# Kernel optimization log

Hardware: AMD Instinct MI355X
Metric: run time of the kernel (lower is better)

Reference implementation:

```python
import jax, jax.numpy as jnp
import numpy as np
from jax import lax

B, N, T, NX = 4, 512, 24, 8
H = 64
PRED_LEN, NY = 12, 1
E_RAND = 8192
EPS = 1e-5


def setup_inputs() -> dict:
    key = jax.random.key(0)
    ks = jax.random.split(key, 24)
    sc = lambda k, shape: (jax.random.normal(k, shape, jnp.float32) * 0.05)
    x = jax.random.normal(ks[0], (B, N, T, NX), jnp.float32)
    er = jax.random.randint(ks[1], (2, E_RAND), 0, N, dtype=jnp.int32)
    loops = jnp.stack([jnp.arange(N, dtype=jnp.int32), jnp.arange(N, dtype=jnp.int32)])
    edge_index = jnp.concatenate([er, loops], axis=1)  # [2, 8704]
    return {
        'x': x,
        'edge_index': edge_index,
        'W_fc': sc(ks[2], (NX, H)), 'b_fc': jnp.zeros((H,), jnp.float32),
        'W1': sc(ks[3], (H, H)), 'a_l1': sc(ks[4], (H,)), 'a_r1': sc(ks[5], (H,)), 'bias1': jnp.zeros((H,), jnp.float32),
        'W2': sc(ks[6], (H, H)), 'a_l2': sc(ks[7], (H,)), 'a_r2': sc(ks[8], (H,)), 'bias2': jnp.zeros((H,), jnp.float32),
        'W_ih': sc(ks[9], (4 * H, H)), 'W_hh': sc(ks[10], (4 * H, H)),
        'b_ih': jnp.zeros((4 * H,), jnp.float32), 'b_hh': jnp.zeros((4 * H,), jnp.float32),
        'g_l': jnp.ones((H,), jnp.float32), 'b_l': jnp.zeros((H,), jnp.float32),
        'g_g': jnp.ones((H,), jnp.float32), 'b_g': jnp.zeros((H,), jnp.float32),
        'W_d': sc(ks[11], (H, PRED_LEN * NY)), 'b_d': jnp.zeros((PRED_LEN * NY,), jnp.float32),
    }


def _layer_norm(x, g, b):
    mu = jnp.mean(x, axis=-1, keepdims=True)
    var = jnp.mean(jnp.square(x - mu), axis=-1, keepdims=True)
    return (x - mu) * lax.rsqrt(var + EPS) * g + b


def _gat(x, W, a_l, a_r, bias, mask):
    # x: [B,N,T,F] -> operate in [B,T,N,H] layout (torch transpose(1,2))
    h = jnp.einsum('bntf,fh->btnh', x, W)          # [B,T,N,H]
    el = jnp.einsum('btnh,h->btn', h, a_l)          # attn_l
    er = jnp.einsum('btnh,h->btn', h, a_r)          # attn_r
    e = el[..., :, None] + er[..., None, :]         # [B,T,N,N]
    e = jax.nn.leaky_relu(e, negative_slope=0.2)
    e = jnp.where(mask, e, -jnp.inf)
    alpha = jax.nn.softmax(e, axis=-1)
    out = jnp.einsum('btmn,btnh->bmth', alpha, h) + bias  # back to [B,N,T,H]
    return jax.nn.gelu(out, approximate=False)


def _lstm(xseq, W_ih, W_hh, b_ih, b_hh):
    # xseq: [M, T, H] -> outputs [M, T, H]; PyTorch gate order i,f,g,o
    M = xseq.shape[0]
    Hh = W_hh.shape[1]
    b = b_ih + b_hh
    def step(carry, xt):
        hprev, cprev = carry
        gates = xt @ W_ih.T + hprev @ W_hh.T + b
        i, f, g, o = jnp.split(gates, 4, axis=-1)
        c = jax.nn.sigmoid(f) * cprev + jax.nn.sigmoid(i) * jnp.tanh(g)
        h = jax.nn.sigmoid(o) * jnp.tanh(c)
        return (h, c), h
    init = (jnp.zeros((M, Hh), xseq.dtype), jnp.zeros((M, Hh), xseq.dtype))
    _, hs = lax.scan(step, init, xseq.transpose(1, 0, 2))  # [T,M,H]
    return hs.transpose(1, 0, 2)


def reference(x, edge_index, W_fc, b_fc, W1, a_l1, a_r1, bias1, W2, a_l2, a_r2, bias2,
              W_ih, W_hh, b_ih, b_hh, g_l, b_l, g_g, b_g, W_d, b_d):
    Bb, Nn, Tt, _ = x.shape
    mask = jnp.zeros((Nn, Nn), bool).at[edge_index[0], edge_index[1]].set(True)
    x_h = jnp.einsum('bntf,fh->bnth', x, W_fc) + b_fc          # fc
    g1 = _gat(x_h, W1, a_l1, a_r1, bias1, mask)                # conv1
    g2 = _gat(g1, W2, a_l2, a_r2, bias2, mask)                 # conv2
    l = _lstm(x_h.reshape(Bb * Nn, Tt, -1), W_ih, W_hh, b_ih, b_hh).reshape(Bb, Nn, Tt, -1)
    h = _layer_norm(g2, g_g, b_g) + _layer_norm(l, g_l, b_l)
    last = h[:, :, -1, :]                                       # [B,N,H]
    out = last @ W_d + b_d                                      # [B,N,pred_len*ny]
    return out.reshape(Bb, Nn, PRED_LEN, NY)
```

## Files before the change

### kernel.cpp

```cpp
#include <hip/hip_runtime.h>
#include <hip/hip_bf16.h>
#include <math.h>

#define BB 4
#define NN 512
#define TT 24
#define NXF 8
#define HH 64
#define PRED 12
#define MM (BB*NN)

typedef __attribute__((ext_vector_type(8))) short short8;
typedef __attribute__((ext_vector_type(4))) float f32x4;
typedef unsigned short ushort;

#define WS_H1THI   0
#define WS_H1TLO   65536
#define WS_H2THI   131072
#define WS_H2TLO   196608
#define WS_HL      262144
#define WS_EL      393216
#define WS_ER      395264
#define WS_EL2     397312
#define WS_ER2     399360
#define WS_WCOMB   401408
#define WS_BCOMB   403456
#define WS_WHHFRAG 403712

#define LHS 72
#define LXS 40

__device__ inline float sigm(float x){ return 1.f/(1.f+__expf(-x)); }
__device__ inline float tanh_fast(float x){ float e=__expf(2.f*x); return 1.f - 2.f/(e+1.f); }
__device__ inline float gelu_exact(float x){ return 0.5f*x*(1.f+erff(x*0.70710678118654752440f)); }
__device__ inline ushort f2bu(float f){
    unsigned b=__float_as_uint(f);
    return (ushort)((b + 0x7FFFu + ((b>>16)&1u))>>16);
}
__device__ inline float bu2f(ushort u){ return __uint_as_float(((unsigned)u)<<16); }

__device__ inline void split8(const float* f, short8& hi, short8& lo){
    #pragma unroll
    for (int j = 0; j < 8; ++j){
        ushort h = f2bu(f[j]);
        hi[j] = (short)h;
        lo[j] = (short)f2bu(f[j] - bu2f(h));
    }
}

__global__ __launch_bounds__(256,2) void gat1pre_kernel(
    const float* __restrict__ x, const float* __restrict__ Wfc, const float* __restrict__ bfc,
    const float* __restrict__ W1, const float* __restrict__ al1, const float* __restrict__ ar1,
    const float* __restrict__ Wih, const float* __restrict__ Whh,
    const float* __restrict__ bih, const float* __restrict__ bhh,
    ushort* __restrict__ H1Thi, ushort* __restrict__ H1Tlo,
    float* __restrict__ el, float* __restrict__ er,
    float* __restrict__ wcombG, float* __restrict__ bcombG,
    ushort* __restrict__ whhfrag)
{
    __shared__ float sw1[HH*HH];
    __shared__ float swfc[NXF*HH];
    __shared__ float sb[HH], sal[HH], sar[HH];
    __shared__ float sxh[4][68];
    __shared__ float sx[4][NXF];
    const int t = threadIdx.x;

    if (blockIdx.x >= 512){
        const int f = blockIdx.x - 512;
        const int ng = t;
        float accf = 0.f, accb = 0.f;
        const float* wr = Wih + ng*64;
        #pragma unroll
        for (int k = 0; k < 64; ++k){
            float wv = wr[k];
            accf += Wfc[f*64 + k] * wv;
            accb += bfc[k] * wv;
        }
        wcombG[f*256 + ng] = accf;
        if (f == 0) bcombG[ng] = accb + bih[ng] + bhh[ng];
        #pragma unroll
        for (int u = 0; u < 8; ++u){
            int o = f*2048 + u*256 + t;
            int F  = o >> 9;
            int ln = (o >> 3) & 63;
            int j  = o & 7;
            int w_ = F >> 3, tt = (F >> 1) & 3, ks = F & 1;
            int q = ln >> 4, c = ln & 15;
            int ngx = (w_ + 4*tt)*16 + c;
            whhfrag[o] = f2bu(Whh[ngx*64 + ks*32 + q*8 + j]);
        }
        return;
    }

    const int r = t >> 6, h = t & 63;
    #pragma unroll
    for (int i = 0; i < 16; ++i) sw1[t + 256*i] = W1[t + 256*i];
    swfc[t] = Wfc[t];
    swfc[t+256] = Wfc[t+256];
    if (t < 64) sb[t] = bfc[t];
    else if (t < 128) sal[t-64] = al1[t-64];
    else if (t < 192) sar[t-128] = ar1[t-128];
    if (t < 32){
        int rr = t >> 3, f = t & 7;
        sx[rr][f] = x[(size_t)(blockIdx.x*4 + rr)*(TT*NXF) + (TT-1)*NXF + f];
    }
    __syncthreads();
    float xh = sb[h];
    #pragma unroll
    for (int f = 0; f < NXF; ++f) xh += sx[r][f]*swfc[f*HH + h];
    sxh[r][h] = xh;
    __syncthreads();
    float acc = 0.f;
    const float4* xr = (const float4*)&sxh[r][0];
    #pragma unroll
    for (int k4 = 0; k4 < 16; ++k4){
        float4 xv = xr[k4];
        acc += xv.x*sw1[(4*k4+0)*HH+h] + xv.y*sw1[(4*k4+1)*HH+h]
             + xv.z*sw1[(4*k4+2)*HH+h] + xv.w*sw1[(4*k4+3)*HH+h];
    }
    const int m = blockIdx.x*4 + r;
    {
        int bb = m >> 9, ml = m & 511;
        ushort hu = f2bu(acc);
        H1Thi[((size_t)(bb*HH + h))*NN + ml] = hu;
        H1Tlo[((size_t)(bb*HH + h))*NN + ml] = f2bu(acc - bu2f(hu));
    }
    float v1 = acc*sal[h], v2 = acc*sar[h];
    #pragma unroll
    for (int o = 32; o; o >>= 1){ v1 += __shfl_xor(v1,o); v2 += __shfl_xor(v2,o); }
    if (h == 0){ el[m] = v1; er[m] = v2; }
}

__global__ __launch_bounds__(256,2) void mid_fused_kernel(
    const ushort* __restrict__ H1Thi, const ushort* __restrict__ H1Tlo,
    const float* __restrict__ el_in, const float* __restrict__ er_in,
    const int* __restrict__ ei, int E,
    const float* __restrict__ bias1,
    const float* __restrict__ W2, const float* __restrict__ al2, const float* __restrict__ ar2,
    ushort* __restrict__ H2Thi, ushort* __restrict__ H2Tlo,
    float* __restrict__ el2, float* __restrict__ er2,
    const float* __restrict__ x,
    const float* __restrict__ wcombG, const float* __restrict__ bcombG,
    const ushort* __restrict__ whhfrag,
    float* __restrict__ hl)
{
    __shared__ __align__(16) char smem[58880];
    const int t = threadIdx.x;
    const int lane = t & 63;
    const int w = t >> 6;
    const int quad = lane >> 4;
    const int c16 = lane & 15;

    if (blockIdx.x >= 128){
        ushort* hbi = (ushort*)smem;
        ushort* hlo = (ushort*)(smem + 4608);
        ushort* xls = (ushort*)(smem + 9216);
        const int m0 = (blockIdx.x - 128) * 16;

        {
            unsigned* h0 = (unsigned*)hbi;
            unsigned* l0 = (unsigned*)hlo;
            for (int i = t; i < 2*16*LHS/2; i += 256){ h0[i] = 0u; l0[i] = 0u; }
            unsigned* xw = (unsigned*)xls;
            for (int i = t; i < TT*16*LXS/2; i += 256) xw[i] = 0u;
        }
        short8 bw[4][2]; short8 bx[4]; float bc[4];
        #pragma unroll
        for (int tt = 0; tt < 4; ++tt){
            const int ng = (w + 4*tt)*16 + c16;
            bc[tt] = bcombG[ng];
            #pragma unroll
            for (int ks = 0; ks < 2; ++ks)
                bw[tt][ks] = *(const short8*)&whhfrag[(((w*4+tt)*2)+ks)*512 + lane*8];
            short8 vx = {0,0,0,0,0,0,0,0};
            if (quad == 0){
                #pragma unroll
                for (int j = 0; j < 8; ++j) vx[j] = (short)f2bu(wcombG[j*256 + ng]);
            }
            bx[tt] = vx;
        }
        __syncthreads();
        for (int i = t; i < 16*TT*NXF; i += 256){
            int r = i / (TT*NXF);
            int rem = i - r*(TT*NXF);
            int st = rem >> 3, f = rem & 7;
            xls[st*(16*LXS) + r*LXS + f] = f2bu(x[(size_t)(m0+r)*(TT*NXF) + rem]);
        }
        __syncthreads();

        float cst[4] = {0,0,0,0};
        float hf[4]  = {0,0,0,0};

        for (int st = 0; st < TT; ++st){
            const int p = st & 1;
            const ushort* hb  = hbi + p*(16*LHS);
            const ushort* hl_ = hlo + p*(16*LHS);
            short8 ahi0 = *(const short8*)&hb[c16*LHS + quad*8];
            short8 ahi1 = *(const short8*)&hb[c16*LHS + 32 + quad*8];
            short8 alo0 = *(const short8*)&hl_[c16*LHS + quad*8];
            short8 alo1 = *(const short8*)&hl_[c16*LHS + 32 + quad*8];
            short8 ax   = *(const short8*)&xls[st*(16*LXS) + c16*LXS + quad*8];
            f32x4 acc[4];
            #pragma unroll
            for (int tt = 0; tt < 4; ++tt){
                f32x4 a = {bc[tt], bc[tt], bc[tt], bc[tt]};
                a = __builtin_amdgcn_mfma_f32_16x16x32_bf16(ax,   bx[tt],    a, 0,0,0);
                a = __builtin_amdgcn_mfma_f32_16x16x32_bf16(ahi0, bw[tt][0], a, 0,0,0);
                a = __builtin_amdgcn_mfma_f32_16x16x32_bf16(ahi1, bw[tt][1], a, 0,0,0);
                a = __builtin_amdgcn_mfma_f32_16x16x32_bf16(alo0, bw[tt][0], a, 0,0,0);
                a = __builtin_amdgcn_mfma_f32_16x16x32_bf16(alo1, bw[tt][1], a, 0,0,0);
                acc[tt] = a;
            }
            ushort* ho   = hbi + (p^1)*(16*LHS);
            ushort* lo_o = hlo + (p^1)*(16*LHS);
            #pragma unroll
            for (int reg = 0; reg < 4; ++reg){
                float gi = acc[0][reg], gf = acc[1][reg], gg = acc[2][reg], go = acc[3][reg];
                float cn = sigm(gf)*cst[reg] + sigm(gi)*tanh_fast(gg);
                cst[reg] = cn;
                float hn = sigm(go)*tanh_fast(cn);
                hf[reg] = hn;
                ushort hu = f2bu(hn);
                float lov = hn - bu2f(hu);
                int addr = (quad*4+reg)*LHS + w*16 + c16;
                ho[addr] = hu;
                lo_o[addr] = f2bu(lov);
            }
            __syncthreads();
        }
        #pragma unroll
        for (int reg = 0; reg < 4; ++reg)
            hl[(size_t)(m0 + quad*4 + reg)*HH + w*16 + c16] = hf[reg];
        return;
    }

    unsigned (*smask)[16] = (unsigned(*)[16])smem;
    float* er_s  = (float*)(smem + 1024);
    float* sal   = (float*)(smem + 3072);
    float* sar   = (float*)(smem + 3328);
    float (*alpha)[516] = (float(*)[516])(smem + 3584);
    float* uSpace = (float*)(smem + 36608);
    float (*xh2)[68] = (float(*)[68])(smem + 54528);

    const int b = blockIdx.x >> 5;
    const int m0 = (blockIdx.x & 31) * 16;
    const int l = lane;

    if (t < 64) sal[t] = al2[t]; else if (t < 128) sar[t-64] = ar2[t-64];
    ((unsigned*)smask)[t] = 0;
    er_s[t] = er_in[b*NN + t];
    er_s[t+256] = er_in[b*NN + t + 256];
    __syncthreads();
    for (int e = t; e < E; e += 256){
        int s = ei[e];
        unsigned rl = (unsigned)(s - m0);
        if (rl < 16u){
            int d = ei[E + e];
            atomicOr(&smask[rl][d>>5], 1u << (d & 31));
        }
    }
    __syncthreads();
    for (int q = 0; q < 4; ++q){
        const int i = w*4 + q;
        const float elv = el_in[b*NN + m0 + i];
        float e8[8]; unsigned mk = 0; float mx = -1e30f;
        #pragma unroll
        for (int j = 0; j < 8; ++j){
            int n = l + 64*j;
            float ev = elv + er_s[n];
            ev = ev >= 0.f ? ev : 0.2f*ev;
            unsigned mb = (smask[i][(l>>5) + 2*j] >> (l & 31)) & 1u;
            e8[j] = ev;
            if (mb){ mk |= (1u<<j); mx = fmaxf(mx, ev); }
        }
        #pragma unroll
        for (int o = 32; o; o >>= 1) mx = fmaxf(mx, __shfl_xor(mx, o));
        float s = 0.f;
        #pragma unroll
        for (int j = 0; j < 8; ++j){
            float p = ((mk>>j) & 1u) ? __expf(e8[j]-mx) : 0.f;
            e8[j] = p; s += p;
        }
        #pragma unroll
        for (int o = 32; o; o >>= 1) s += __shfl_xor(s, o);
        const float inv = 1.f/s;
        #pragma unroll
        for (int j = 0; j < 8; ++j) alpha[i][l + 64*j] = e8[j]*inv;
    }
    __syncthreads();

    const ushort* bhp = H1Thi + ((size_t)(b*HH + w*16 + c16))*NN;
    const ushort* blp = H1Tlo + ((size_t)(b*HH + w*16 + c16))*NN;
    f32x4 acc = {0.f,0.f,0.f,0.f};
    for (int k0 = 0; k0 < NN; k0 += 32){
        const float* ap = &alpha[c16][k0 + quad*8];
        float4 a0 = *(const float4*)ap;
        float4 a1 = *(const float4*)(ap + 4);
        float af[8] = {a0.x,a0.y,a0.z,a0.w,a1.x,a1.y,a1.z,a1.w};
        short8 a_h, a_l;
        split8(af, a_h, a_l);
        short8 b_h = *(const short8*)&bhp[k0 + quad*8];
        short8 b_l = *(const short8*)&blp[k0 + quad*8];
        acc = __builtin_amdgcn_mfma_f32_16x16x32_bf16(a_h, b_h, acc, 0,0,0);
        acc = __builtin_amdgcn_mfma_f32_16x16x32_bf16(a_l, b_h, acc, 0,0,0);
        acc = __builtin_amdgcn_mfma_f32_16x16x32_bf16(a_h, b_l, acc, 0,0,0);
    }
    __syncthreads();
    {
        const int h = w*16 + c16;
        const float bv = bias1[h];
        #pragma unroll
        for (int reg = 0; reg < 4; ++reg)
            xh2[quad*4 + reg][h] = gelu_exact(acc[reg] + bv);
    }
    float* sw2 = uSpace;
    #pragma unroll
    for (int i = 0; i < 16; ++i) sw2[t + 256*i] = W2[t + 256*i];
    __syncthreads();
    {
        const int h = l;
        for (int q = 0; q < 4; ++q){
            const int i = w + 4*q;
            float acc2 = 0.f;
            const float4* xr = (const float4*)&xh2[i][0];
            #pragma unroll
            for (int k4 = 0; k4 < 16; ++k4){
                float4 xv = xr[k4];
                acc2 += xv.x*sw2[(4*k4+0)*HH+h] + xv.y*sw2[(4*k4+1)*HH+h]
                      + xv.z*sw2[(4*k4+2)*HH+h] + xv.w*sw2[(4*k4+3)*HH+h];
            }
            const int m = b*NN + m0 + i;
            ushort hu = f2bu(acc2);
            H2Thi[((size_t)(b*HH + h))*NN + (m0 + i)] = hu;
            H2Tlo[((size_t)(b*HH + h))*NN + (m0 + i)] = f2bu(acc2 - bu2f(hu));
            float v1 = acc2*sal[h], v2 = acc2*sar[h];
            #pragma unroll
            for (int o = 32; o; o >>= 1){ v1 += __shfl_xor(v1,o); v2 += __shfl_xor(v2,o); }
            if (h == 0){ el2[m] = v1; er2[m] = v2; }
        }
    }
}

__global__ __launch_bounds__(256,2) void attn2_final_kernel(
    const ushort* __restrict__ H2Thi, const ushort* __restrict__ H2Tlo,
    const float* __restrict__ el_in, const float* __restrict__ er_in,
    const int* __restrict__ ei, int E,
    const float* __restrict__ bias2,
    const float* __restrict__ hl,
    const float* __restrict__ g_l, const float* __restrict__ b_l,
    const float* __restrict__ g_g, const float* __restrict__ b_g,
    const float* __restrict__ W_d, const float* __restrict__ b_d,
    float* __restrict__ out)
{
    __shared__ __align__(16) char smem[54016];
    unsigned (*smask)[16] = (unsigned(*)[16])smem;
    float* er_s  = (float*)(smem + 1024);
    float (*alpha)[516] = (float(*)[516])(smem + 3072);

    const int t = threadIdx.x;
    const int b = blockIdx.x >> 5;
    const int m0 = (blockIdx.x & 31) * 16;
    const int l = t & 63, w = t >> 6;
    const int quad = l >> 4, c16 = l & 15;

    ((unsigned*)smask)[t] = 0;
    er_s[t] = er_in[b*NN + t];
    er_s[t+256] = er_in[b*NN + t + 256];
    __syncthreads();
    for (int e = t; e < E; e += 256){
        int s = ei[e];
        unsigned rl = (unsigned)(s - m0);
        if (rl < 16u){
            int d = ei[E + e];
            atomicOr(&smask[rl][d>>5], 1u << (d & 31));
        }
    }
    __syncthreads();
    for (int q = 0; q < 4; ++q){
        const int i = w*4 + q;
        const float elv = el_in[b*NN + m0 + i];
        float e8[8]; unsigned mk = 0; float mx = -1e30f;
        #pragma unroll
        for (int j = 0; j < 8; ++j){
            int n = l + 64*j;
            float ev = elv + er_s[n];
            ev = ev >= 0.f ? ev : 0.2f*ev;
            unsigned mb = (smask[i][(l>>5) + 2*j] >> (l & 31)) & 1u;
            e8[j] = ev;
            if (mb){ mk |= (1u<<j); mx = fmaxf(mx, ev); }
        }
        #pragma unroll
        for (int o = 32; o; o >>= 1) mx = fmaxf(mx, __shfl_xor(mx, o));
        float s = 0.f;
        #pragma unroll
        for (int j = 0; j < 8; ++j){
            float p = ((mk>>j) & 1u) ? __expf(e8[j]-mx) : 0.f;
            e8[j] = p; s += p;
        }
        #pragma unroll
        for (int o = 32; o; o >>= 1) s += __shfl_xor(s, o);
        const float inv = 1.f/s;
        #pragma unroll
        for (int j = 0; j < 8; ++j) alpha[i][l + 64*j] = e8[j]*inv;
    }
    __syncthreads();

    const ushort* bhp = H2Thi + ((size_t)(b*HH + w*16 + c16))*NN;
    const ushort* blp = H2Tlo + ((size_t)(b*HH + w*16 + c16))*NN;
    f32x4 acc = {0.f,0.f,0.f,0.f};
    for (int k0 = 0; k0 < NN; k0 += 32){
        const float* ap = &alpha[c16][k0 + quad*8];
        float4 a0 = *(const float4*)ap;
        float4 a1 = *(const float4*)(ap + 4);
        float af[8] = {a0.x,a0.y,a0.z,a0.w,a1.x,a1.y,a1.z,a1.w};
        short8 a_h, a_l;
        split8(af, a_h, a_l);
        short8 b_h = *(const short8*)&bhp[k0 + quad*8];
        short8 b_l = *(const short8*)&blp[k0 + quad*8];
        acc = __builtin_amdgcn_mfma_f32_16x16x32_bf16(a_h, b_h, acc, 0,0,0);
        acc = __builtin_amdgcn_mfma_f32_16x16x32_bf16(a_l, b_h, acc, 0,0,0);
        acc = __builtin_amdgcn_mfma_f32_16x16x32_bf16(a_h, b_l, acc, 0,0,0);
    }
    __syncthreads();
    float* sg2  = (float*)(smem + 3072);
    float* sdec = (float*)(smem + 36096);
    {
        const int h = w*16 + c16;
        const float bv = bias2[h];
        #pragma unroll
        for (int reg = 0; reg < 4; ++reg)
            sg2[(quad*4 + reg)*HH + h] = gelu_exact(acc[reg] + bv);
    }
    __syncthreads();
    const int gbase = b*NN + m0;
    {
        const int h = l;
        for (int q = 0; q < 4; ++q){
            const int ml = w*4 + q;
            float gv = sg2[ml*HH + h];
            float lv = hl[(size_t)(gbase + ml)*HH + h];

            float s1 = gv;
            #pragma unroll
            for (int o = 32; o; o >>= 1) s1 += __shfl_xor(s1, o);
            float dg = gv - s1*(1.f/64.f);
            float v1 = dg*dg;
            #pragma unroll
            for (int o = 32; o; o >>= 1) v1 += __shfl_xor(v1, o);
            float lng = dg*rsqrtf(v1*(1.f/64.f) + 1e-5f)*g_g[h] + b_g[h];

            float s2 = lv;
            #pragma unroll
            for (int o = 32; o; o >>= 1) s2 += __shfl_xor(s2, o);
            float dl = lv - s2*(1.f/64.f);
            float v2 = dl*dl;
            #pragma unroll
            for (int o = 32; o; o >>= 1) v2 += __shfl_xor(v2, o);
            float lnl = dl*rsqrtf(v2*(1.f/64.f) + 1e-5f)*g_l[h] + b_l[h];

            sdec[ml*HH + h] = lng + lnl;
        }
    }
    __syncthreads();
    if (t < 16*PRED){
        int rr = t / PRED, pp = t - rr*PRED;
        float a = b_d[pp];
        #pragma unroll
        for (int k = 0; k < HH; ++k) a += sdec[rr*HH + k]*W_d[k*PRED + pp];
        out[(size_t)(gbase + rr)*PRED + pp] = a;
    }
}

extern "C" void kernel_launch(void* const* d_in, const int* in_sizes, int n_in,
                              void* d_out, int out_size, void* d_ws, size_t ws_size,
                              hipStream_t stream){
    const float* x    = (const float*)d_in[0];
    const int*   ei   = (const int*)  d_in[1];
    const float* Wfc  = (const float*)d_in[2];
    const float* bfc  = (const float*)d_in[3];
    const float* W1   = (const float*)d_in[4];
    const float* al1  = (const float*)d_in[5];
    const float* ar1  = (const float*)d_in[6];
    const float* bias1= (const float*)d_in[7];
    const float* W2   = (const float*)d_in[8];
    const float* al2  = (const float*)d_in[9];
    const float* ar2  = (const float*)d_in[10];
    const float* bias2= (const float*)d_in[11];
    const float* Wih  = (const float*)d_in[12];
    const float* Whh  = (const float*)d_in[13];
    const float* bih  = (const float*)d_in[14];
    const float* bhh  = (const float*)d_in[15];
    const float* g_l  = (const float*)d_in[16];
    const float* b_l  = (const float*)d_in[17];
    const float* g_g  = (const float*)d_in[18];
    const float* b_g  = (const float*)d_in[19];
    const float* W_d  = (const float*)d_in[20];
    const float* b_d  = (const float*)d_in[21];

    float* ws = (float*)d_ws;
    const int E = in_sizes[1] / 2;

    gat1pre_kernel<<<512 + 8, 256, 0, stream>>>(x, Wfc, bfc, W1, al1, ar1,
                                                Wih, Whh, bih, bhh,
                                                (ushort*)(ws+WS_H1THI), (ushort*)(ws+WS_H1TLO),
                                                ws+WS_EL, ws+WS_ER,
                                                ws+WS_WCOMB, ws+WS_BCOMB,
                                                (ushort*)(ws+WS_WHHFRAG));
    mid_fused_kernel<<<256, 256, 0, stream>>>((const ushort*)(ws+WS_H1THI), (const ushort*)(ws+WS_H1TLO),
                                              ws+WS_EL, ws+WS_ER,
                                              ei, E, bias1, W2, al2, ar2,
                                              (ushort*)(ws+WS_H2THI), (ushort*)(ws+WS_H2TLO),
                                              ws+WS_EL2, ws+WS_ER2,
                                              x, ws+WS_WCOMB, ws+WS_BCOMB,
                                              (const ushort*)(ws+WS_WHHFRAG),
                                              ws+WS_HL);
    attn2_final_kernel<<<BB*(NN/16), 256, 0, stream>>>((const ushort*)(ws+WS_H2THI), (const ushort*)(ws+WS_H2TLO),
                                                       ws+WS_EL2, ws+WS_ER2,
                                                       ei, E, bias2,
                                                       ws+WS_HL,
                                                       g_l, b_l, g_g, b_g, W_d, b_d,
                                                       (float*)d_out);
}
```

Baseline: 151.2 us.

## Merge three kernels into one cooperative kernel with grid syncs

Replaces the three separate launches (GAT1 projection, mid-stage LSTM/attention, final attention and decoder) with a single cooperative mega-kernel of 256 blocks that uses grid.sync between phases. The first phase now handles 8 rows per block, and the last 8 blocks also precompute the combined LSTM weights. The aim is to remove kernel launch gaps and inter-kernel drain costs. In exchange it adds grid-wide barriers and requires all 256 blocks to be co-resident. The LSTM blocks may also stall the grid at the second sync.

```diff
diff --git a/kernel.cpp b/kernel.cpp
--- a/kernel.cpp
+++ b/kernel.cpp
@@ -1,6 +1,9 @@
 #include <hip/hip_runtime.h>
+#include <hip/hip_cooperative_groups.h>
 #include <hip/hip_bf16.h>
 #include <math.h>
+
+namespace cg = cooperative_groups;
 
 #define BB 4
 #define NN 512
@@ -48,150 +51,129 @@
     }
 }
 
-__global__ __launch_bounds__(256,2) void gat1pre_kernel(
-    const float* __restrict__ x, const float* __restrict__ Wfc, const float* __restrict__ bfc,
-    const float* __restrict__ W1, const float* __restrict__ al1, const float* __restrict__ ar1,
-    const float* __restrict__ Wih, const float* __restrict__ Whh,
-    const float* __restrict__ bih, const float* __restrict__ bhh,
-    ushort* __restrict__ H1Thi, ushort* __restrict__ H1Tlo,
-    float* __restrict__ el, float* __restrict__ er,
-    float* __restrict__ wcombG, float* __restrict__ bcombG,
-    ushort* __restrict__ whhfrag)
-{
-    __shared__ float sw1[HH*HH];
-    __shared__ float swfc[NXF*HH];
-    __shared__ float sb[HH], sal[HH], sar[HH];
-    __shared__ float sxh[4][68];
-    __shared__ float sx[4][NXF];
-    const int t = threadIdx.x;
-
-    if (blockIdx.x >= 512){
-        const int f = blockIdx.x - 512;
-        const int ng = t;
-        float accf = 0.f, accb = 0.f;
-        const float* wr = Wih + ng*64;
-        #pragma unroll
-        for (int k = 0; k < 64; ++k){
-            float wv = wr[k];
-            accf += Wfc[f*64 + k] * wv;
-            accb += bfc[k] * wv;
-        }
-        wcombG[f*256 + ng] = accf;
-        if (f == 0) bcombG[ng] = accb + bih[ng] + bhh[ng];
-        #pragma unroll
-        for (int u = 0; u < 8; ++u){
-            int o = f*2048 + u*256 + t;
-            int F  = o >> 9;
-            int ln = (o >> 3) & 63;
-            int j  = o & 7;
-            int w_ = F >> 3, tt = (F >> 1) & 3, ks = F & 1;
-            int q = ln >> 4, c = ln & 15;
-            int ngx = (w_ + 4*tt)*16 + c;
-            whhfrag[o] = f2bu(Whh[ngx*64 + ks*32 + q*8 + j]);
-        }
-        return;
+struct Params {
+    const float *x; const int *ei; int E;
+    const float *Wfc,*bfc,*W1,*al1,*ar1,*bias1,*W2,*al2,*ar2,*bias2;
+    const float *Wih,*Whh,*bih,*bhh,*g_l,*b_l,*g_g,*b_g,*W_d,*b_d;
+    ushort *H1Thi,*H1Tlo,*H2Thi,*H2Tlo;
+    float *hl,*el,*er,*el2,*er2,*wcombG,*bcombG; ushort *whhfrag;
+    float *out;
+};
+
+__global__ __launch_bounds__(256,2) void mega_kernel(Params P){
+    __shared__ __align__(16) char smem[41344];
+    cg::grid_group grid = cg::this_grid();
+    const int t = threadIdx.x, blk = blockIdx.x;
+    const int lane = t & 63, w = t >> 6, quad = lane >> 4, c16 = lane & 15;
+
+    {
+        float* sw1  = (float*)smem;
+        float* swfc = (float*)(smem+16384);
+        float* sb   = (float*)(smem+18432);
+        float* sal  = (float*)(smem+18688);
+        float* sar  = (float*)(smem+18944);
+        float (*sx)[8]   = (float(*)[8])(smem+19200);
+        float (*sxh)[68] = (float(*)[68])(smem+19456);
+
+        #pragma unroll
+        for (int i=0;i<16;++i) sw1[t+256*i] = P.W1[t+256*i];
+        swfc[t] = P.Wfc[t]; swfc[t+256] = P.Wfc[t+256];
+        if (t<64) sb[t]=P.bfc[t];
+        else if (t<128) sal[t-64]=P.al1[t-64];
+        else if (t<192) sar[t-128]=P.ar1[t-128];
+        if (t<64){ int rr=t>>3, f=t&7;
+            sx[rr][f] = P.x[(size_t)(blk*8+rr)*(TT*NXF) + (TT-1)*NXF + f]; }
+        __syncthreads();
+        const int r = t>>6, h = t&63;
+        #pragma unroll
+        for (int p=0;p<2;++p){
+            int row = p*4+r;
+            float xh = sb[h];
+            #pragma unroll
+            for (int f=0; f<NXF; ++f) xh += sx[row][f]*swfc[f*HH+h];
+            sxh[row][h] = xh;
+        }
+        __syncthreads();
+        #pragma unroll
+        for (int p=0;p<2;++p){
+            int row = p*4+r; int m = blk*8+row;
+            float acc = 0.f;
+            const float4* xr = (const float4*)&sxh[row][0];
+            #pragma unroll
+            for (int k4=0;k4<16;++k4){
+                float4 xv = xr[k4];
+                acc += xv.x*sw1[(4*k4+0)*HH+h] + xv.y*sw1[(4*k4+1)*HH+h]
+                     + xv.z*sw1[(4*k4+2)*HH+h] + xv.w*sw1[(4*k4+3)*HH+h];
+            }
+            int bb = m >> 9, ml = m & 511;
+            ushort hu = f2bu(acc);
+            P.H1Thi[((size_t)(bb*HH + h))*NN + ml] = hu;
+            P.H1Tlo[((size_t)(bb*HH + h))*NN + ml] = f2bu(acc - bu2f(hu));
+            float v1 = acc*sal[h], v2 = acc*sar[h];
+            #pragma unroll
+            for (int o=32;o;o>>=1){ v1 += __shfl_xor(v1,o); v2 += __shfl_xor(v2,o); }
+            if (h==0){ P.el[m]=v1; P.er[m]=v2; }
+        }
+        if (blk >= 248){
+            const int f = blk-248, ng = t;
+            float accf=0.f, accb=0.f;
+            const float* wr = P.Wih + ng*64;
+            #pragma unroll
+            for (int k=0;k<64;++k){ float wv=wr[k]; accf += P.Wfc[f*64+k]*wv; accb += P.bfc[k]*wv; }
+            P.wcombG[f*256+ng] = accf;
+            if (f==0) P.bcombG[ng] = accb + P.bih[ng] + P.bhh[ng];
+            #pragma unroll
+            for (int u=0;u<8;++u){
+                int o = f*2048 + u*256 + t;
+                int F = o>>9, ln=(o>>3)&63, j=o&7;
+                int w_=F>>3, tt=(F>>1)&3, ks=F&1;
+                int q=ln>>4, c=ln&15;
+                int ngx=(w_+4*tt)*16 + c;
+                P.whhfrag[o] = f2bu(P.Whh[ngx*64 + ks*32 + q*8 + j]);
+            }
+        }
     }
-
-    const int r = t >> 6, h = t & 63;
-    #pragma unroll
-    for (int i = 0; i < 16; ++i) sw1[t + 256*i] = W1[t + 256*i];
-    swfc[t] = Wfc[t];
-    swfc[t+256] = Wfc[t+256];
-    if (t < 64) sb[t] = bfc[t];
-    else if (t < 128) sal[t-64] = al1[t-64];
-    else if (t < 192) sar[t-128] = ar1[t-128];
-    if (t < 32){
-        int rr = t >> 3, f = t & 7;
-        sx[rr][f] = x[(size_t)(blockIdx.x*4 + rr)*(TT*NXF) + (TT-1)*NXF + f];
-    }
-    __syncthreads();
-    float xh = sb[h];
-    #pragma unroll
-    for (int f = 0; f < NXF; ++f) xh += sx[r][f]*swfc[f*HH + h];
-    sxh[r][h] = xh;
-    __syncthreads();
-    float acc = 0.f;
-    const float4* xr = (const float4*)&sxh[r][0];
-    #pragma unroll
-    for (int k4 = 0; k4 < 16; ++k4){
-        float4 xv = xr[k4];
-        acc += xv.x*sw1[(4*k4+0)*HH+h] + xv.y*sw1[(4*k4+1)*HH+h]
-             + xv.z*sw1[(4*k4+2)*HH+h] + xv.w*sw1[(4*k4+3)*HH+h];
-    }
-    const int m = blockIdx.x*4 + r;
-    {
-        int bb = m >> 9, ml = m & 511;
-        ushort hu = f2bu(acc);
-        H1Thi[((size_t)(bb*HH + h))*NN + ml] = hu;
-        H1Tlo[((size_t)(bb*HH + h))*NN + ml] = f2bu(acc - bu2f(hu));
-    }
-    float v1 = acc*sal[h], v2 = acc*sar[h];
-    #pragma unroll
-    for (int o = 32; o; o >>= 1){ v1 += __shfl_xor(v1,o); v2 += __shfl_xor(v2,o); }
-    if (h == 0){ el[m] = v1; er[m] = v2; }
-}
-
-__global__ __launch_bounds__(256,2) void mid_fused_kernel(
-    const ushort* __restrict__ H1Thi, const ushort* __restrict__ H1Tlo,
-    const float* __restrict__ el_in, const float* __restrict__ er_in,
-    const int* __restrict__ ei, int E,
-    const float* __restrict__ bias1,
-    const float* __restrict__ W2, const float* __restrict__ al2, const float* __restrict__ ar2,
-    ushort* __restrict__ H2Thi, ushort* __restrict__ H2Tlo,
-    float* __restrict__ el2, float* __restrict__ er2,
-    const float* __restrict__ x,
-    const float* __restrict__ wcombG, const float* __restrict__ bcombG,
-    const ushort* __restrict__ whhfrag,
-    float* __restrict__ hl)
-{
-    __shared__ __align__(16) char smem[58880];
-    const int t = threadIdx.x;
-    const int lane = t & 63;
-    const int w = t >> 6;
-    const int quad = lane >> 4;
-    const int c16 = lane & 15;
-
-    if (blockIdx.x >= 128){
+    grid.sync();
+
+    if (blk >= 128){
         ushort* hbi = (ushort*)smem;
-        ushort* hlo = (ushort*)(smem + 4608);
-        ushort* xls = (ushort*)(smem + 9216);
-        const int m0 = (blockIdx.x - 128) * 16;
-
+        ushort* hlo = (ushort*)(smem+4608);
+        ushort* xls = (ushort*)(smem+9216);
+        const int m0 = (blk-128)*16;
         {
             unsigned* h0 = (unsigned*)hbi;
             unsigned* l0 = (unsigned*)hlo;
-            for (int i = t; i < 2*16*LHS/2; i += 256){ h0[i] = 0u; l0[i] = 0u; }
+            for (int i=t;i<2*16*LHS/2;i+=256){ h0[i]=0u; l0[i]=0u; }
             unsigned* xw = (unsigned*)xls;
-            for (int i = t; i < TT*16*LXS/2; i += 256) xw[i] = 0u;
+            for (int i=t;i<TT*16*LXS/2;i+=256) xw[i]=0u;
         }
         short8 bw[4][2]; short8 bx[4]; float bc[4];
         #pragma unroll
-        for (int tt = 0; tt < 4; ++tt){
+        for (int tt=0;tt<4;++tt){
             const int ng = (w + 4*tt)*16 + c16;
-            bc[tt] = bcombG[ng];
-            #pragma unroll
-            for (int ks = 0; ks < 2; ++ks)
-                bw[tt][ks] = *(const short8*)&whhfrag[(((w*4+tt)*2)+ks)*512 + lane*8];
+            bc[tt] = P.bcombG[ng];
+            #pragma unroll
+            for (int ks=0;ks<2;++ks)
+                bw[tt][ks] = *(const short8*)&P.whhfrag[(((w*4+tt)*2)+ks)*512 + lane*8];
             short8 vx = {0,0,0,0,0,0,0,0};
             if (quad == 0){
                 #pragma unroll
-                for (int j = 0; j < 8; ++j) vx[j] = (short)f2bu(wcombG[j*256 + ng]);
+                for (int j=0;j<8;++j) vx[j] = (short)f2bu(P.wcombG[j*256 + ng]);
             }
             bx[tt] = vx;
         }
         __syncthreads();
-        for (int i = t; i < 16*TT*NXF; i += 256){
-            int r = i / (TT*NXF);
+        for (int i=t;i<16*TT*NXF;i+=256){
+            int r = i/(TT*NXF);
             int rem = i - r*(TT*NXF);
-            int st = rem >> 3, f = rem & 7;
-            xls[st*(16*LXS) + r*LXS + f] = f2bu(x[(size_t)(m0+r)*(TT*NXF) + rem]);
+            int st = rem>>3, f = rem&7;
+            xls[st*(16*LXS) + r*LXS + f] = f2bu(P.x[(size_t)(m0+r)*(TT*NXF) + rem]);
         }
         __syncthreads();
 
         float cst[4] = {0,0,0,0};
         float hf[4]  = {0,0,0,0};
-
-        for (int st = 0; st < TT; ++st){
+        for (int st=0; st<TT; ++st){
             const int p = st & 1;
             const ushort* hb  = hbi + p*(16*LHS);
             const ushort* hl_ = hlo + p*(16*LHS);
@@ -202,7 +184,7 @@
             short8 ax   = *(const short8*)&xls[st*(16*LXS) + c16*LXS + quad*8];
             f32x4 acc[4];
             #pragma unroll
-            for (int tt = 0; tt < 4; ++tt){
+            for (int tt=0;tt<4;++tt){
                 f32x4 a = {bc[tt], bc[tt], bc[tt], bc[tt]};
                 a = __builtin_amdgcn_mfma_f32_16x16x32_bf16(ax,   bx[tt],    a, 0,0,0);
                 a = __builtin_amdgcn_mfma_f32_16x16x32_bf16(ahi0, bw[tt][0], a, 0,0,0);
@@ -214,7 +196,7 @@
             ushort* ho   = hbi + (p^1)*(16*LHS);
             ushort* lo_o = hlo + (p^1)*(16*LHS);
             #pragma unroll
-            for (int reg = 0; reg < 4; ++reg){
+            for (int reg=0;reg<4;++reg){
                 float gi = acc[0][reg], gf = acc[1][reg], gg = acc[2][reg], go = acc[3][reg];
                 float cn = sigm(gf)*cst[reg] + sigm(gi)*tanh_fast(gg);
                 cst[reg] = cn;
@@ -229,295 +211,264 @@
             __syncthreads();
         }
         #pragma unroll
-        for (int reg = 0; reg < 4; ++reg)
-            hl[(size_t)(m0 + quad*4 + reg)*HH + w*16 + c16] = hf[reg];
-        return;
+        for (int reg=0;reg<4;++reg)
+            P.hl[(size_t)(m0 + quad*4 + reg)*HH + w*16 + c16] = hf[reg];
+    } else {
+        unsigned (*smask)[16] = (unsigned(*)[16])smem;
+        float* er_s = (float*)(smem+1024);
+        float* sal  = (float*)(smem+3072);
+        float* sar  = (float*)(smem+3328);
+        float (*alpha)[516] = (float(*)[516])(smem+3584);
+        float (*xh2)[68] = (float(*)[68])(smem+36608);
+
+        const int b = blk>>5, m0 = (blk&31)*16;
+        const int l = lane;
+        if (t < 64) sal[t] = P.al2[t]; else if (t < 128) sar[t-64] = P.ar2[t-64];
+        ((unsigned*)smask)[t] = 0;
+        er_s[t] = P.er[b*NN+t];
+        er_s[t+256] = P.er[b*NN+t+256];
+        __syncthreads();
+        for (int e=t;e<P.E;e+=256){
+            int s = P.ei[e];
+            unsigned rl = (unsigned)(s-m0);
+            if (rl<16u){ int d = P.ei[P.E+e]; atomicOr(&smask[rl][d>>5], 1u<<(d&31)); }
+        }
+        __syncthreads();
+        for (int q=0;q<4;++q){
+            const int i = w*4+q;
+            const float elv = P.el[b*NN+m0+i];
+            float e8[8]; unsigned mk=0; float mx=-1e30f;
+            #pragma unroll
+            for (int j=0;j<8;++j){
+                int n = l + 64*j;
+                float ev = elv + er_s[n];
+                ev = ev >= 0.f ? ev : 0.2f*ev;
+                unsigned mb = (smask[i][(l>>5) + 2*j] >> (l&31)) & 1u;
+                e8[j] = ev;
+                if (mb){ mk |= (1u<<j); mx = fmaxf(mx, ev); }
+            }
+            #pragma unroll
+            for (int o=32;o;o>>=1) mx = fmaxf(mx, __shfl_xor(mx,o));
+            float s = 0.f;
+            #pragma unroll
+            for (int j=0;j<8;++j){
+                float pp = ((mk>>j)&1u) ? __expf(e8[j]-mx) : 0.f;
+                e8[j] = pp; s += pp;
+            }
+            #pragma unroll
+            for (int o=32;o;o>>=1) s += __shfl_xor(s,o);
+            const float inv = 1.f/s;
+            #pragma unroll
+            for (int j=0;j<8;++j) alpha[i][l + 64*j] = e8[j]*inv;
+        }
+        __syncthreads();
+        const ushort* bhp = P.H1Thi + ((size_t)(b*HH + w*16 + c16))*NN;
+        const ushort* blp = P.H1Tlo + ((size_t)(b*HH + w*16 + c16))*NN;
+        f32x4 acc = {0.f,0.f,0.f,0.f};
+        for (int k0=0;k0<NN;k0+=32){
+            const float* ap = &alpha[c16][k0 + quad*8];
+            float4 a0 = *(const float4*)ap;
+            float4 a1 = *(const float4*)(ap + 4);
+            float af[8] = {a0.x,a0.y,a0.z,a0.w,a1.x,a1.y,a1.z,a1.w};
+            short8 a_h, a_l;
+            split8(af, a_h, a_l);
+            short8 b_h = *(const short8*)&bhp[k0 + quad*8];
+            short8 b_l = *(const short8*)&blp[k0 + quad*8];
+            acc = __builtin_amdgcn_mfma_f32_16x16x32_bf16(a_h, b_h, acc, 0,0,0);
+            acc = __builtin_amdgcn_mfma_f32_16x16x32_bf16(a_l, b_h, acc, 0,0,0);
+            acc = __builtin_amdgcn_mfma_f32_16x16x32_bf16(a_h, b_l, acc, 0,0,0);
+        }
+        __syncthreads();
+        {
+            const int h = w*16 + c16;
+            const float bv = P.bias1[h];
+            #pragma unroll
+            for (int reg=0;reg<4;++reg)
+                xh2[quad*4+reg][h] = gelu_exact(acc[reg]+bv);
+        }
+        float* sw2 = (float*)(smem+3584);
+        #pragma unroll
+        for (int i=0;i<16;++i) sw2[t+256*i] = P.W2[t+256*i];
+        __syncthreads();
+        {
+            const int h = l;
+            for (int q=0;q<4;++q){
+                const int i = w + 4*q;
+                float acc2 = 0.f;
+                const float4* xr = (const float4*)&xh2[i][0];
+                #pragma unroll
+                for (int k4=0;k4<16;++k4){
+                    float4 xv = xr[k4];
+                    acc2 += xv.x*sw2[(4*k4+0)*HH+h] + xv.y*sw2[(4*k4+1)*HH+h]
+                          + xv.z*sw2[(4*k4+2)*HH+h] + xv.w*sw2[(4*k4+3)*HH+h];
+                }
+                const int m = b*NN + m0 + i;
+                ushort hu = f2bu(acc2);
+                P.H2Thi[((size_t)(b*HH+h))*NN + (m0+i)] = hu;
+                P.H2Tlo[((size_t)(b*HH+h))*NN + (m0+i)] = f2bu(acc2 - bu2f(hu));
+                float v1 = acc2*sal[h], v2 = acc2*sar[h];
+                #pragma unroll
+                for (int o=32;o;o>>=1){ v1 += __shfl_xor(v1,o); v2 += __shfl_xor(v2,o); }
+                if (h==0){ P.el2[m]=v1; P.er2[m]=v2; }
+            }
+        }
     }
-
-    unsigned (*smask)[16] = (unsigned(*)[16])smem;
-    float* er_s  = (float*)(smem + 1024);
-    float* sal   = (float*)(smem + 3072);
-    float* sar   = (float*)(smem + 3328);
-    float (*alpha)[516] = (float(*)[516])(smem + 3584);
-    float* uSpace = (float*)(smem + 36608);
-    float (*xh2)[68] = (float(*)[68])(smem + 54528);
-
-    const int b = blockIdx.x >> 5;
-    const int m0 = (blockIdx.x & 31) * 16;
-    const int l = lane;
-
-    if (t < 64) sal[t] = al2[t]; else if (t < 128) sar[t-64] = ar2[t-64];
-    ((unsigned*)smask)[t] = 0;
-    er_s[t] = er_in[b*NN + t];
-    er_s[t+256] = er_in[b*NN + t + 256];
-    __syncthreads();
-    for (int e = t; e < E; e += 256){
-        int s = ei[e];
-        unsigned rl = (unsigned)(s - m0);
-        if (rl < 16u){
-            int d = ei[E + e];
-            atomicOr(&smask[rl][d>>5], 1u << (d & 31));
-        }
-    }
-    __syncthreads();
-    for (int q = 0; q < 4; ++q){
-        const int i = w*4 + q;
-        const float elv = el_in[b*NN + m0 + i];
-        float e8[8]; unsigned mk = 0; float mx = -1e30f;
-        #pragma unroll
-        for (int j = 0; j < 8; ++j){
-            int n = l + 64*j;
-            float ev = elv + er_s[n];
-            ev = ev >= 0.f ? ev : 0.2f*ev;
-            unsigned mb = (smask[i][(l>>5) + 2*j] >> (l & 31)) & 1u;
-            e8[j] = ev;
-            if (mb){ mk |= (1u<<j); mx = fmaxf(mx, ev); }
-        }
-        #pragma unroll
-        for (int o = 32; o; o >>= 1) mx = fmaxf(mx, __shfl_xor(mx, o));
-        float s = 0.f;
-        #pragma unroll
-        for (int j = 0; j < 8; ++j){
-            float p = ((mk>>j) & 1u) ? __expf(e8[j]-mx) : 0.f;
-            e8[j] = p; s += p;
-        }
-        #pragma unroll
-        for (int o = 32; o; o >>= 1) s += __shfl_xor(s, o);
-        const float inv = 1.f/s;
-        #pragma unroll
-        for (int j = 0; j < 8; ++j) alpha[i][l + 64*j] = e8[j]*inv;
-    }
-    __syncthreads();
-
-    const ushort* bhp = H1Thi + ((size_t)(b*HH + w*16 + c16))*NN;
-    const ushort* blp = H1Tlo + ((size_t)(b*HH + w*16 + c16))*NN;
-    f32x4 acc = {0.f,0.f,0.f,0.f};
-    for (int k0 = 0; k0 < NN; k0 += 32){
-        const float* ap = &alpha[c16][k0 + quad*8];
-        float4 a0 = *(const float4*)ap;
-        float4 a1 = *(const float4*)(ap + 4);
-        float af[8] = {a0.x,a0.y,a0.z,a0.w,a1.x,a1.y,a1.z,a1.w};
-        short8 a_h, a_l;
-        split8(af, a_h, a_l);
-        short8 b_h = *(const short8*)&bhp[k0 + quad*8];
-        short8 b_l = *(const short8*)&blp[k0 + quad*8];
-        acc = __builtin_amdgcn_mfma_f32_16x16x32_bf16(a_h, b_h, acc, 0,0,0);
-        acc = __builtin_amdgcn_mfma_f32_16x16x32_bf16(a_l, b_h, acc, 0,0,0);
-        acc = __builtin_amdgcn_mfma_f32_16x16x32_bf16(a_h, b_l, acc, 0,0,0);
-    }
-    __syncthreads();
-    {
-        const int h = w*16 + c16;
-        const float bv = bias1[h];
-        #pragma unroll
-        for (int reg = 0; reg < 4; ++reg)
-            xh2[quad*4 + reg][h] = gelu_exact(acc[reg] + bv);
-    }
-    float* sw2 = uSpace;
-    #pragma unroll
-    for (int i = 0; i < 16; ++i) sw2[t + 256*i] = W2[t + 256*i];
-    __syncthreads();
-    {
-        const int h = l;
-        for (int q = 0; q < 4; ++q){
-            const int i = w + 4*q;
-            float acc2 = 0.f;
-            const float4* xr = (const float4*)&xh2[i][0];
-            #pragma unroll
-            for (int k4 = 0; k4 < 16; ++k4){
-                float4 xv = xr[k4];
-                acc2 += xv.x*sw2[(4*k4+0)*HH+h] + xv.y*sw2[(4*k4+1)*HH+h]
-                      + xv.z*sw2[(4*k4+2)*HH+h] + xv.w*sw2[(4*k4+3)*HH+h];
-            }
-            const int m = b*NN + m0 + i;
-            ushort hu = f2bu(acc2);
-            H2Thi[((size_t)(b*HH + h))*NN + (m0 + i)] = hu;
-            H2Tlo[((size_t)(b*HH + h))*NN + (m0 + i)] = f2bu(acc2 - bu2f(hu));
-            float v1 = acc2*sal[h], v2 = acc2*sar[h];
-            #pragma unroll
-            for (int o = 32; o; o >>= 1){ v1 += __shfl_xor(v1,o); v2 += __shfl_xor(v2,o); }
-            if (h == 0){ el2[m] = v1; er2[m] = v2; }
-        }
-    }
-}
-
-__global__ __launch_bounds__(256,2) void attn2_final_kernel(
-    const ushort* __restrict__ H2Thi, const ushort* __restrict__ H2Tlo,
-    const float* __restrict__ el_in, const float* __restrict__ er_in,
-    const int* __restrict__ ei, int E,
-    const float* __restrict__ bias2,
-    const float* __restrict__ hl,
-    const float* __restrict__ g_l, const float* __restrict__ b_l,
-    const float* __restrict__ g_g, const float* __restrict__ b_g,
-    const float* __restrict__ W_d, const float* __restrict__ b_d,
-    float* __restrict__ out)
-{
-    __shared__ __align__(16) char smem[54016];
-    unsigned (*smask)[16] = (unsigned(*)[16])smem;
-    float* er_s  = (float*)(smem + 1024);
-    float (*alpha)[516] = (float(*)[516])(smem + 3072);
-
-    const int t = threadIdx.x;
-    const int b = blockIdx.x >> 5;
-    const int m0 = (blockIdx.x & 31) * 16;
-    const int l = t & 63, w = t >> 6;
-    const int quad = l >> 4, c16 = l & 15;
-
-    ((unsigned*)smask)[t] = 0;
-    er_s[t] = er_in[b*NN + t];
-    er_s[t+256] = er_in[b*NN + t + 256];
-    __syncthreads();
-    for (int e = t; e < E; e += 256){
-        int s = ei[e];
-        unsigned rl = (unsigned)(s - m0);
-        if (rl < 16u){
-            int d = ei[E + e];
-            atomicOr(&smask[rl][d>>5], 1u << (d & 31));
-        }
-    }
-    __syncthreads();
-    for (int q = 0; q < 4; ++q){
-        const int i = w*4 + q;
-        const float elv = el_in[b*NN + m0 + i];
-        float e8[8]; unsigned mk = 0; float mx = -1e30f;
-        #pragma unroll
-        for (int j = 0; j < 8; ++j){
-            int n = l + 64*j;
-            float ev = elv + er_s[n];
-            ev = ev >= 0.f ? ev : 0.2f*ev;
-            unsigned mb = (smask[i][(l>>5) + 2*j] >> (l & 31)) & 1u;
-            e8[j] = ev;
-            if (mb){ mk |= (1u<<j); mx = fmaxf(mx, ev); }
-        }
-        #pragma unroll
-        for (int o = 32; o; o >>= 1) mx = fmaxf(mx, __shfl_xor(mx, o));
-        float s = 0.f;
-        #pragma unroll
-        for (int j = 0; j < 8; ++j){
-            float p = ((mk>>j) & 1u) ? __expf(e8[j]-mx) : 0.f;
-            e8[j] = p; s += p;
-        }
-        #pragma unroll
-        for (int o = 32; o; o >>= 1) s += __shfl_xor(s, o);
-        const float inv = 1.f/s;
-        #pragma unroll
-        for (int j = 0; j < 8; ++j) alpha[i][l + 64*j] = e8[j]*inv;
-    }
-    __syncthreads();
-
-    const ushort* bhp = H2Thi + ((size_t)(b*HH + w*16 + c16))*NN;
-    const ushort* blp = H2Tlo + ((size_t)(b*HH + w*16 + c16))*NN;
-    f32x4 acc = {0.f,0.f,0.f,0.f};
-    for (int k0 = 0; k0 < NN; k0 += 32){
-        const float* ap = &alpha[c16][k0 + quad*8];
-        float4 a0 = *(const float4*)ap;
-        float4 a1 = *(const float4*)(ap + 4);
-        float af[8] = {a0.x,a0.y,a0.z,a0.w,a1.x,a1.y,a1.z,a1.w};
-        short8 a_h, a_l;
-        split8(af, a_h, a_l);
-        short8 b_h = *(const short8*)&bhp[k0 + quad*8];
-        short8 b_l = *(const short8*)&blp[k0 + quad*8];
-        acc = __builtin_amdgcn_mfma_f32_16x16x32_bf16(a_h, b_h, acc, 0,0,0);
-        acc = __builtin_amdgcn_mfma_f32_16x16x32_bf16(a_l, b_h, acc, 0,0,0);
-        acc = __builtin_amdgcn_mfma_f32_16x16x32_bf16(a_h, b_l, acc, 0,0,0);
-    }
-    __syncthreads();
-    float* sg2  = (float*)(smem + 3072);
-    float* sdec = (float*)(smem + 36096);
-    {
-        const int h = w*16 + c16;
-        const float bv = bias2[h];
-        #pragma unroll
-        for (int reg = 0; reg < 4; ++reg)
-            sg2[(quad*4 + reg)*HH + h] = gelu_exact(acc[reg] + bv);
-    }
-    __syncthreads();
-    const int gbase = b*NN + m0;
-    {
-        const int h = l;
-        for (int q = 0; q < 4; ++q){
-            const int ml = w*4 + q;
-            float gv = sg2[ml*HH + h];
-            float lv = hl[(size_t)(gbase + ml)*HH + h];
-
-            float s1 = gv;
-            #pragma unroll
-            for (int o = 32; o; o >>= 1) s1 += __shfl_xor(s1, o);
-            float dg = gv - s1*(1.f/64.f);
-            float v1 = dg*dg;
-            #pragma unroll
-            for (int o = 32; o; o >>= 1) v1 += __shfl_xor(v1, o);
-            float lng = dg*rsqrtf(v1*(1.f/64.f) + 1e-5f)*g_g[h] + b_g[h];
-
-            float s2 = lv;
-            #pragma unroll
-            for (int o = 32; o; o >>= 1) s2 += __shfl_xor(s2, o);
-            float dl = lv - s2*(1.f/64.f);
-            float v2 = dl*dl;
-            #pragma unroll
-            for (int o = 32; o; o >>= 1) v2 += __shfl_xor(v2, o);
-            float lnl = dl*rsqrtf(v2*(1.f/64.f) + 1e-5f)*g_l[h] + b_l[h];
-
-            sdec[ml*HH + h] = lng + lnl;
-        }
-    }
-    __syncthreads();
-    if (t < 16*PRED){
-        int rr = t / PRED, pp = t - rr*PRED;
-        float a = b_d[pp];
-        #pragma unroll
-        for (int k = 0; k < HH; ++k) a += sdec[rr*HH + k]*W_d[k*PRED + pp];
-        out[(size_t)(gbase + rr)*PRED + pp] = a;
+    grid.sync();
+
+    if (blk < 128){
+        unsigned (*smask)[16] = (unsigned(*)[16])smem;
+        float* er_s = (float*)(smem+1024);
+        float (*alpha)[516] = (float(*)[516])(smem+3584);
+
+        const int b = blk>>5, m0 = (blk&31)*16;
+        const int l = lane;
+        ((unsigned*)smask)[t] = 0;
+        er_s[t] = P.er2[b*NN+t];
+        er_s[t+256] = P.er2[b*NN+t+256];
+        __syncthreads();
+        for (int e=t;e<P.E;e+=256){
+            int s = P.ei[e];
+            unsigned rl = (unsigned)(s-m0);
+            if (rl<16u){ int d = P.ei[P.E+e]; atomicOr(&smask[rl][d>>5], 1u<<(d&31)); }
+        }
+        __syncthreads();
+        for (int q=0;q<4;++q){
+            const int i = w*4+q;
+            const float elv = P.el2[b*NN+m0+i];
+            float e8[8]; unsigned mk=0; float mx=-1e30f;
+            #pragma unroll
+            for (int j=0;j<8;++j){
+                int n = l + 64*j;
+                float ev = elv + er_s[n];
+                ev = ev >= 0.f ? ev : 0.2f*ev;
+                unsigned mb = (smask[i][(l>>5) + 2*j] >> (l&31)) & 1u;
+                e8[j] = ev;
+                if (mb){ mk |= (1u<<j); mx = fmaxf(mx, ev); }
+            }
+            #pragma unroll
+            for (int o=32;o;o>>=1) mx = fmaxf(mx, __shfl_xor(mx,o));
+            float s = 0.f;
+            #pragma unroll
+            for (int j=0;j<8;++j){
+                float pp = ((mk>>j)&1u) ? __expf(e8[j]-mx) : 0.f;
+                e8[j] = pp; s += pp;
+            }
+            #pragma unroll
+            for (int o=32;o;o>>=1) s += __shfl_xor(s,o);
+            const float inv = 1.f/s;
+            #pragma unroll
+            for (int j=0;j<8;++j) alpha[i][l + 64*j] = e8[j]*inv;
+        }
+        __syncthreads();
+        const ushort* bhp = P.H2Thi + ((size_t)(b*HH + w*16 + c16))*NN;
+        const ushort* blp = P.H2Tlo + ((size_t)(b*HH + w*16 + c16))*NN;
+        f32x4 acc = {0.f,0.f,0.f,0.f};
+        for (int k0=0;k0<NN;k0+=32){
+            const float* ap = &alpha[c16][k0 + quad*8];
+            float4 a0 = *(const float4*)ap;
+            float4 a1 = *(const float4*)(ap + 4);
+            float af[8] = {a0.x,a0.y,a0.z,a0.w,a1.x,a1.y,a1.z,a1.w};
+            short8 a_h, a_l;
+            split8(af, a_h, a_l);
+            short8 b_h = *(const short8*)&bhp[k0 + quad*8];
+            short8 b_l = *(const short8*)&blp[k0 + quad*8];
+            acc = __builtin_amdgcn_mfma_f32_16x16x32_bf16(a_h, b_h, acc, 0,0,0);
+            acc = __builtin_amdgcn_mfma_f32_16x16x32_bf16(a_l, b_h, acc, 0,0,0);
+            acc = __builtin_amdgcn_mfma_f32_16x16x32_bf16(a_h, b_l, acc, 0,0,0);
+        }
+        __syncthreads();
+        float* sg2  = (float*)(smem+3584);
+        float* sdec = (float*)(smem+20224);
+        {
+            const int h = w*16 + c16;
+            const float bv = P.bias2[h];
+            #pragma unroll
+            for (int reg=0;reg<4;++reg)
+                sg2[(quad*4+reg)*HH + h] = gelu_exact(acc[reg]+bv);
+        }
+        __syncthreads();
+        const int gbase = b*NN + m0;
+        {
+            const int h = l;
+            for (int q=0;q<4;++q){
+                const int ml = w*4+q;
+                float gv = sg2[ml*HH+h];
+                float lv = P.hl[(size_t)(gbase+ml)*HH + h];
+
+                float s1 = gv;
+                #pragma unroll
+                for (int o=32;o;o>>=1) s1 += __shfl_xor(s1,o);
+                float dg = gv - s1*(1.f/64.f);
+                float v1 = dg*dg;
+                #pragma unroll
+                for (int o=32;o;o>>=1) v1 += __shfl_xor(v1,o);
+                float lng = dg*rsqrtf(v1*(1.f/64.f)+1e-5f)*P.g_g[h] + P.b_g[h];
+
+                float s2 = lv;
+                #pragma unroll
+                for (int o=32;o;o>>=1) s2 += __shfl_xor(s2,o);
+                float dl = lv - s2*(1.f/64.f);
+                float v2 = dl*dl;
+                #pragma unroll
+                for (int o=32;o;o>>=1) v2 += __shfl_xor(v2,o);
+                float lnl = dl*rsqrtf(v2*(1.f/64.f)+1e-5f)*P.g_l[h] + P.b_l[h];
+
+                sdec[ml*HH+h] = lng + lnl;
+            }
+        }
+        __syncthreads();
+        if (t < 16*PRED){
+            int rr = t/PRED, pp = t - rr*PRED;
+            float a = P.b_d[pp];
+            #pragma unroll
+            for (int k=0;k<HH;++k) a += sdec[rr*HH+k]*P.W_d[k*PRED+pp];
+            P.out[(size_t)(gbase+rr)*PRED+pp] = a;
+        }
     }
 }
 
 extern "C" void kernel_launch(void* const* d_in, const int* in_sizes, int n_in,
                               void* d_out, int out_size, void* d_ws, size_t ws_size,
                               hipStream_t stream){
-    const float* x    = (const float*)d_in[0];
-    const int*   ei   = (const int*)  d_in[1];
-    const float* Wfc  = (const float*)d_in[2];
-    const float* bfc  = (const float*)d_in[3];
-    const float* W1   = (const float*)d_in[4];
-    const float* al1  = (const float*)d_in[5];
-    const float* ar1  = (const float*)d_in[6];
-    const float* bias1= (const float*)d_in[7];
-    const float* W2   = (const float*)d_in[8];
-    const float* al2  = (const float*)d_in[9];
-    const float* ar2  = (const float*)d_in[10];
-    const float* bias2= (const float*)d_in[11];
-    const float* Wih  = (const float*)d_in[12];
-    const float* Whh  = (const float*)d_in[13];
-    const float* bih  = (const float*)d_in[14];
-    const float* bhh  = (const float*)d_in[15];
-    const float* g_l  = (const float*)d_in[16];
-    const float* b_l  = (const float*)d_in[17];
-    const float* g_g  = (const float*)d_in[18];
-    const float* b_g  = (const float*)d_in[19];
-    const float* W_d  = (const float*)d_in[20];
-    const float* b_d  = (const float*)d_in[21];
-
     float* ws = (float*)d_ws;
-    const int E = in_sizes[1] / 2;
-
-    gat1pre_kernel<<<512 + 8, 256, 0, stream>>>(x, Wfc, bfc, W1, al1, ar1,
-                                                Wih, Whh, bih, bhh,
-                                                (ushort*)(ws+WS_H1THI), (ushort*)(ws+WS_H1TLO),
-                                                ws+WS_EL, ws+WS_ER,
-                                                ws+WS_WCOMB, ws+WS_BCOMB,
-                                                (ushort*)(ws+WS_WHHFRAG));
-    mid_fused_kernel<<<256, 256, 0, stream>>>((const ushort*)(ws+WS_H1THI), (const ushort*)(ws+WS_H1TLO),
-                                              ws+WS_EL, ws+WS_ER,
-                                              ei, E, bias1, W2, al2, ar2,
-                                              (ushort*)(ws+WS_H2THI), (ushort*)(ws+WS_H2TLO),
-                                              ws+WS_EL2, ws+WS_ER2,
-                                              x, ws+WS_WCOMB, ws+WS_BCOMB,
-                                              (const ushort*)(ws+WS_WHHFRAG),
-                                              ws+WS_HL);
-    attn2_final_kernel<<<BB*(NN/16), 256, 0, stream>>>((const ushort*)(ws+WS_H2THI), (const ushort*)(ws+WS_H2TLO),
-                                                       ws+WS_EL2, ws+WS_ER2,
-                                                       ei, E, bias2,
-                                                       ws+WS_HL,
-                                                       g_l, b_l, g_g, b_g, W_d, b_d,
-                                                       (float*)d_out);
+    Params prm;
+    prm.x    = (const float*)d_in[0];
+    prm.ei   = (const int*)  d_in[1];
+    prm.E    = in_sizes[1]/2;
+    prm.Wfc  = (const float*)d_in[2];
+    prm.bfc  = (const float*)d_in[3];
+    prm.W1   = (const float*)d_in[4];
+    prm.al1  = (const float*)d_in[5];
+    prm.ar1  = (const float*)d_in[6];
+    prm.bias1= (const float*)d_in[7];
+    prm.W2   = (const float*)d_in[8];
+    prm.al2  = (const float*)d_in[9];
+    prm.ar2  = (const float*)d_in[10];
+    prm.bias2= (const float*)d_in[11];
+    prm.Wih  = (const float*)d_in[12];
+    prm.Whh  = (const float*)d_in[13];
+    prm.bih  = (const float*)d_in[14];
+    prm.bhh  = (const float*)d_in[15];
+    prm.g_l  = (const float*)d_in[16];
+    prm.b_l  = (const float*)d_in[17];
+    prm.g_g  = (const float*)d_in[18];
+    prm.b_g  = (const float*)d_in[19];
+    prm.W_d  = (const float*)d_in[20];
+    prm.b_d  = (const float*)d_in[21];
+    prm.H1Thi = (ushort*)(ws + WS_H1THI);
+    prm.H1Tlo = (ushort*)(ws + WS_H1TLO);
+    prm.H2Thi = (ushort*)(ws + WS_H2THI);
+    prm.H2Tlo = (ushort*)(ws + WS_H2TLO);
+    prm.hl    = ws + WS_HL;
+    prm.el    = ws + WS_EL;
+    prm.er    = ws + WS_ER;
+    prm.el2   = ws + WS_EL2;
+    prm.er2   = ws + WS_ER2;
+    prm.wcombG= ws + WS_WCOMB;
+    prm.bcombG= ws + WS_BCOMB;
+    prm.whhfrag = (ushort*)(ws + WS_WHHFRAG);
+    prm.out   = (float*)d_out;
+
+    void* args[] = { &prm };
+    hipLaunchCooperativeKernel((void*)mega_kernel, dim3(256), dim3(256), args, 0, stream);
 }
```

Measured after the change: 246.4 us. 62.9% more time.
